# Kernel optimization log

Measured on AMD Instinct MI355X. Metric: run time of the kernel, lower is better.

Reference implementation:

```python
import jax, jax.numpy as jnp
import numpy as np

N_NODES = 500000
N_EDGES = 16000000
IN_DIM = 17


def setup_inputs() -> dict:
    key = jax.random.key(0)
    k1, k2, k3, k4, k5, k6, k7 = jax.random.split(key, 7)
    x = jax.random.normal(k1, (N_NODES, IN_DIM), dtype=jnp.float32)
    edge_index = jax.random.randint(k2, (2, N_EDGES), 0, N_NODES, dtype=jnp.int64)
    edge_weight = jax.random.uniform(k3, (N_EDGES,), dtype=jnp.float32)
    # SAGEConv(17, 1): lin_l applied to aggregated neighbors (with bias),
    # lin_r applied to root features (no bias, PyG convention).
    s = 1.0 / np.sqrt(IN_DIM)
    w_l = jax.random.uniform(k4, (1, IN_DIM), minval=-s, maxval=s, dtype=jnp.float32)
    b_l = jax.random.uniform(k5, (1,), minval=-s, maxval=s, dtype=jnp.float32)
    w_r = jax.random.uniform(k6, (1, IN_DIM), minval=-s, maxval=s, dtype=jnp.float32)
    # out: Linear(1, 1)
    k8, k9 = jax.random.split(k7)
    w_o = jax.random.uniform(k8, (1, 1), minval=-1.0, maxval=1.0, dtype=jnp.float32)
    b_o = jax.random.uniform(k9, (1,), minval=-1.0, maxval=1.0, dtype=jnp.float32)
    return {"x": x, "edge_index": edge_index, "edge_weight": edge_weight,
            "w_l": w_l, "b_l": b_l, "w_r": w_r, "w_o": w_o, "b_o": b_o}


def reference(x, edge_index, edge_weight, w_l, b_l, w_r, w_o, b_o):
    # SAGEConv (mean aggregation). edge_weight is unused (faithful to PyG SAGEConv).
    # Project to out_dim=1 BEFORE aggregation (linearity makes this exact and
    # avoids materializing a [E,17] gathered buffer):
    #   lin_l(mean_j x_j) + b_l == mean_j (x_j @ W_l^T) + b_l
    src, dst = edge_index[0], edge_index[1]
    x_proj_l = x @ w_l.T                      # [N, 1]
    msg = x_proj_l[src, 0]                    # [E]  gathered source projections
    agg = jax.ops.segment_sum(msg, dst, num_segments=x.shape[0])          # [N]
    cnt = jax.ops.segment_sum(jnp.ones_like(msg), dst, num_segments=x.shape[0])
    mean = agg / jnp.maximum(cnt, 1.0)        # zero for isolated nodes
    h = mean[:, None] + b_l + x @ w_r.T       # [N, 1]  lin_l(aggr) + lin_r(x)
    h = jax.nn.elu(h)
    return h @ w_o.T + b_o                    # [N, 1]
```

## Files before the change

### kernel.cpp

```cpp
#include <hip/hip_runtime.h>
#include <hip/hip_bf16.h>
#include <math.h>

#define IN_DIM 17
#define NB 128
#define LOG_BN 12
#define BN 4096
#define K_SPLIT 8
#define GRP 8
#define CHUNK 8192
#define EPT 32
#define VAL_SCALE 4096.0f
#define FP_SCALE 268435456.0f
#define FP_INV   (1.0 / 268435456.0)

__global__ void node_proj_kernel(const float* __restrict__ x,
                                 const float* __restrict__ w_l,
                                 const float* __restrict__ w_r,
                                 float* __restrict__ p_l,
                                 float* __restrict__ p_r,
                                 int n_nodes) {
    int i = blockIdx.x * blockDim.x + threadIdx.x;
    if (i >= n_nodes) return;
    const float* row = x + (size_t)i * IN_DIM;
    float sl = 0.0f, sr = 0.0f;
#pragma unroll
    for (int k = 0; k < IN_DIM; ++k) {
        float v = row[k];
        sl = fmaf(v, w_l[k], sl);
        sr = fmaf(v, w_r[k], sr);
    }
    p_l[i] = sl;
    p_r[i] = sr;
}

__global__ __launch_bounds__(256, 4)
void sort_scatter_kernel(const int* __restrict__ src,
                         const int* __restrict__ dst,
                         const float* __restrict__ p_l,
                         unsigned* __restrict__ staging,
                         unsigned short* __restrict__ segtab,
                         int n_edges) {
    __shared__ unsigned cnt[NB];
    __shared__ unsigned sstart[NB + 1];
    __shared__ unsigned lbuf[CHUNK];

    const int tid = threadIdx.x;
    const int blk = blockIdx.x;
    const int e0 = blk * CHUNK;
    const int chunk_n = min(CHUNK, n_edges - e0);
    const int nvec = chunk_n >> 2;

    for (int t = tid; t < NB; t += 256) cnt[t] = 0;
    __syncthreads();

    uint4 dreg[EPT / 4];
    uint4 sreg[EPT / 4];
    unsigned rpack[EPT / 2];
    const uint4* dv = (const uint4*)(dst + e0);
    const uint4* sv = (const uint4*)(src + e0);
#pragma unroll
    for (int k = 0; k < EPT / 4; ++k) {
        int q = tid + k * 256;
        if (q < nvec) {
            uint4 d = dv[q];
            dreg[k] = d;
            sreg[k] = sv[q];
            unsigned r0 = atomicAdd(&cnt[d.x >> LOG_BN], 1u);
            unsigned r1 = atomicAdd(&cnt[d.y >> LOG_BN], 1u);
            unsigned r2 = atomicAdd(&cnt[d.z >> LOG_BN], 1u);
            unsigned r3 = atomicAdd(&cnt[d.w >> LOG_BN], 1u);
            rpack[2 * k]     = r0 | (r1 << 16);
            rpack[2 * k + 1] = r2 | (r3 << 16);
        }
    }
    unsigned tail_rank = 0;
    {
        int i = (nvec << 2) + tid;
        if (i < chunk_n)
            tail_rank = atomicAdd(&cnt[(unsigned)dst[e0 + i] >> LOG_BN], 1u);
    }
    __syncthreads();

    if (tid < 64) {
        unsigned c0 = cnt[tid], c1 = cnt[tid + 64];
        unsigned s0 = c0;
#pragma unroll
        for (int off = 1; off < 64; off <<= 1) {
            unsigned v = __shfl_up(s0, off);
            if (tid >= off) s0 += v;
        }
        unsigned tot0 = __shfl(s0, 63);
        unsigned s1 = c1;
#pragma unroll
        for (int off = 1; off < 64; off <<= 1) {
            unsigned v = __shfl_up(s1, off);
            if (tid >= off) s1 += v;
        }
        s1 += tot0;
        sstart[tid + 1] = s0;
        sstart[tid + 65] = s1;
        if (tid == 0) sstart[0] = 0;
    }
    __syncthreads();

    for (int t = tid; t <= NB; t += 256)
        segtab[(size_t)blk * (NB + 2) + t] = (unsigned short)sstart[t];

#pragma unroll
    for (int k = 0; k < EPT / 4; ++k) {
        int q = tid + k * 256;
        if (q < nvec) {
            uint4 s = sreg[k];
            uint4 d = dreg[k];
            float pf[4] = {p_l[s.x], p_l[s.y], p_l[s.z], p_l[s.w]};
            unsigned dd[4] = {d.x, d.y, d.z, d.w};
            unsigned rk[4] = {rpack[2 * k] & 0xFFFFu, rpack[2 * k] >> 16,
                              rpack[2 * k + 1] & 0xFFFFu, rpack[2 * k + 1] >> 16};
#pragma unroll
            for (int u = 0; u < 4; ++u) {
                int fx = __float2int_rn(pf[u] * VAL_SCALE);
                fx = max(-32768, min(32767, fx));
                unsigned entry = ((unsigned)(fx & 0xFFFF) << 16) | (dd[u] & (BN - 1));
                unsigned b = dd[u] >> LOG_BN;
                lbuf[sstart[b] + rk[u]] = entry;
            }
        }
    }
    {
        int i = (nvec << 2) + tid;
        if (i < chunk_n) {
            unsigned s = (unsigned)src[e0 + i];
            unsigned d = (unsigned)dst[e0 + i];
            int fx = __float2int_rn(p_l[s] * VAL_SCALE);
            fx = max(-32768, min(32767, fx));
            unsigned entry = ((unsigned)(fx & 0xFFFF) << 16) | (d & (BN - 1));
            lbuf[sstart[d >> LOG_BN] + tail_rank] = entry;
        }
    }
    __syncthreads();

    uint4* outp = (uint4*)(staging + (size_t)blk * CHUNK);
    const uint4* lp = (const uint4*)lbuf;
    int nv4 = (chunk_n + 3) >> 2;
    for (int q = tid; q < nv4; q += 256)
        outp[q] = lp[q];
}

__global__ __launch_bounds__(256, 4)
void reduce_kernel(const unsigned* __restrict__ staging,
                   const unsigned short* __restrict__ segtab,
                   unsigned* __restrict__ bins,
                   int nblk) {
    __shared__ unsigned lds_p[BN];
    const int tid = threadIdx.x;
    const int b = blockIdx.x / K_SPLIT;
    const int j = blockIdx.x % K_SPLIT;
    const int grp = tid >> 3;
    const int sub = tid & (GRP - 1);

    for (int i = tid; i < BN; i += 256) lds_p[i] = 0u;
    __syncthreads();

    const int c0 = (int)((long long)nblk * j / K_SPLIT);
    const int c1 = (int)((long long)nblk * (j + 1) / K_SPLIT);

    int c = c0 + grp;
    unsigned s_nxt = 0, e_nxt = 0;
    if (c < c1) {
        const unsigned short* st = segtab + (size_t)c * (NB + 2) + b;
        s_nxt = st[0]; e_nxt = st[1];
    }
    while (c < c1) {
        unsigned s = s_nxt, e = e_nxt;
        const int cn = c + 32;
        if (cn < c1) {
            const unsigned short* st = segtab + (size_t)cn * (NB + 2) + b;
            s_nxt = st[0]; e_nxt = st[1];
        }
        const unsigned* sp = staging + (size_t)c * CHUNK;
        for (unsigned i = s + sub; i < e; i += GRP) {
            unsigned en = sp[i];
            int v = (int)(short)(en >> 16);
            atomicAdd(&lds_p[en & (BN - 1)], ((unsigned)v << 8) | 1u);
        }
        c = cn;
    }
    __syncthreads();
    unsigned* gb = bins + (size_t)b * BN;
    for (int i = tid; i < BN; i += 256) {
        unsigned v = lds_p[i];
        if (v) atomicAdd(&gb[i], v);
    }
}

__global__ void finalize_kernel(const float* __restrict__ p_r,
                                const unsigned* __restrict__ bins,
                                const float* __restrict__ b_l,
                                const float* __restrict__ w_o,
                                const float* __restrict__ b_o,
                                float* __restrict__ out,
                                int n_nodes) {
    int i = blockIdx.x * blockDim.x + threadIdx.x;
    if (i >= n_nodes) return;
    unsigned u = bins[i];
    int sum24 = ((int)u) >> 8;
    int cnt = (int)(u & 0xFFu);
    float sum = (float)sum24 * (1.0f / VAL_SCALE);
    float mean = sum / fmaxf((float)cnt, 1.0f);
    float h = mean + b_l[0] + p_r[i];
    h = (h > 0.0f) ? h : expm1f(h);
    out[i] = fmaf(h, w_o[0], b_o[0]);
}

__global__ void edge_scatter_fb(const int* __restrict__ edge_index,
                                const float* __restrict__ p_l,
                                unsigned long long* __restrict__ bins,
                                int n_edges) {
    int e = blockIdx.x * blockDim.x + threadIdx.x;
    if (e >= n_edges) return;
    int s = edge_index[e];
    int d = edge_index[n_edges + e];
    float p = p_l[s];
    long long sfx = (long long)llrintf(p * FP_SCALE);
    unsigned long long delta = ((unsigned long long)sfx << 20) | 1ULL;
    atomicAdd(&bins[d], delta);
}

__global__ void finalize_fb(const float* __restrict__ p_r,
                            const unsigned long long* __restrict__ bins,
                            const float* __restrict__ b_l,
                            const float* __restrict__ w_o,
                            const float* __restrict__ b_o,
                            float* __restrict__ out,
                            int n_nodes) {
    int i = blockIdx.x * blockDim.x + threadIdx.x;
    if (i >= n_nodes) return;
    long long packed = (long long)bins[i];
    int cntv = (int)(packed & 0xFFFFFLL);
    long long sfx = packed >> 20;
    float sum = (float)((double)sfx * FP_INV);
    float mean = sum / fmaxf((float)cntv, 1.0f);
    float h = mean + b_l[0] + p_r[i];
    h = (h > 0.0f) ? h : expm1f(h);
    out[i] = fmaf(h, w_o[0], b_o[0]);
}

static inline size_t align_up(size_t v, size_t a) { return (v + a - 1) & ~(a - 1); }

extern "C" void kernel_launch(void* const* d_in, const int* in_sizes, int n_in,
                              void* d_out, int out_size, void* d_ws, size_t ws_size,
                              hipStream_t stream) {
    const float* x   = (const float*)d_in[0];
    const int*   ei  = (const int*)d_in[1];
    const float* w_l = (const float*)d_in[3];
    const float* b_l = (const float*)d_in[4];
    const float* w_r = (const float*)d_in[5];
    const float* w_o = (const float*)d_in[6];
    const float* b_o = (const float*)d_in[7];
    float* out = (float*)d_out;

    const int n_nodes = in_sizes[0] / IN_DIM;
    const int n_edges = in_sizes[2];
    const int* src = ei;
    const int* dst = ei + n_edges;
    const int nblk = (n_edges + CHUNK - 1) / CHUNK;

    char* ws = (char*)d_ws;
    size_t off = 0;
    size_t o_pl = off;      off = align_up(off + (size_t)n_nodes * 4, 256);
    size_t o_pr = off;      off = align_up(off + (size_t)n_nodes * 4, 256);
    size_t o_stage = off;   off = align_up(off + (size_t)nblk * CHUNK * 4, 256);
    size_t o_seg = off;     off = align_up(off + (size_t)nblk * (NB + 2) * 2, 256);
    size_t o_bins = off;    off = align_up(off + (size_t)NB * BN * 4, 256);
    size_t need = off;

    float* p_l = (float*)(ws + o_pl);
    float* p_r = (float*)(ws + o_pr);

    const int B = 256;
    node_proj_kernel<<<(n_nodes + B - 1) / B, B, 0, stream>>>(x, w_l, w_r, p_l, p_r, n_nodes);

    if (ws_size >= need) {
        unsigned* staging       = (unsigned*)(ws + o_stage);
        unsigned short* segtab  = (unsigned short*)(ws + o_seg);
        unsigned* bins          = (unsigned*)(ws + o_bins);

        hipMemsetAsync(bins, 0, (size_t)NB * BN * 4, stream);
        sort_scatter_kernel<<<nblk, B, 0, stream>>>(src, dst, p_l, staging, segtab, n_edges);
        reduce_kernel<<<NB * K_SPLIT, B, 0, stream>>>(staging, segtab, bins, nblk);
        finalize_kernel<<<(n_nodes + B - 1) / B, B, 0, stream>>>(p_r, bins, b_l, w_o, b_o,
                                                                 out, n_nodes);
    } else {
        unsigned long long* bins_fb = (unsigned long long*)(ws + o_stage);
        hipMemsetAsync(bins_fb, 0, (size_t)n_nodes * 8, stream);
        edge_scatter_fb<<<(n_edges + B - 1) / B, B, 0, stream>>>(ei, p_l, bins_fb, n_edges);
        finalize_fb<<<(n_nodes + B - 1) / B, B, 0, stream>>>(p_r, bins_fb, b_l, w_o, b_o,
                                                             out, n_nodes);
    }
}
```

Measured before the change: 343.2 us.

## Split sort-scatter into separate histogram and scatter kernels

Splits the fused counting-sort kernel in two. A lightweight histogram kernel writes per-block bucket offsets to segtab, and a scatter kernel then reads them and claims slots with LDS atomics. This drops the per-edge rank registers and the in-kernel prefix scan from the scatter pass, which should lower register pressure. In exchange, dst is read twice from global memory and an extra launch is added.

```diff
diff --git a/kernel.cpp b/kernel.cpp
--- a/kernel.cpp
+++ b/kernel.cpp
@@ -34,16 +34,12 @@
     p_r[i] = sr;
 }
 
-__global__ __launch_bounds__(256, 4)
-void sort_scatter_kernel(const int* __restrict__ src,
-                         const int* __restrict__ dst,
-                         const float* __restrict__ p_l,
-                         unsigned* __restrict__ staging,
-                         unsigned short* __restrict__ segtab,
-                         int n_edges) {
-    __shared__ unsigned cnt[NB];
+__global__ __launch_bounds__(256, 8)
+void hist_kernel(const int* __restrict__ dst,
+                 unsigned short* __restrict__ segtab,
+                 int n_edges) {
+    __shared__ unsigned hist[NB];
     __shared__ unsigned sstart[NB + 1];
-    __shared__ unsigned lbuf[CHUNK];
 
     const int tid = threadIdx.x;
     const int blk = blockIdx.x;
@@ -51,39 +47,27 @@
     const int chunk_n = min(CHUNK, n_edges - e0);
     const int nvec = chunk_n >> 2;
 
-    for (int t = tid; t < NB; t += 256) cnt[t] = 0;
-    __syncthreads();
-
-    uint4 dreg[EPT / 4];
-    uint4 sreg[EPT / 4];
-    unsigned rpack[EPT / 2];
+    for (int t = tid; t < NB; t += 256) hist[t] = 0;
+    __syncthreads();
+
     const uint4* dv = (const uint4*)(dst + e0);
-    const uint4* sv = (const uint4*)(src + e0);
 #pragma unroll
     for (int k = 0; k < EPT / 4; ++k) {
         int q = tid + k * 256;
         if (q < nvec) {
             uint4 d = dv[q];
-            dreg[k] = d;
-            sreg[k] = sv[q];
-            unsigned r0 = atomicAdd(&cnt[d.x >> LOG_BN], 1u);
-            unsigned r1 = atomicAdd(&cnt[d.y >> LOG_BN], 1u);
-            unsigned r2 = atomicAdd(&cnt[d.z >> LOG_BN], 1u);
-            unsigned r3 = atomicAdd(&cnt[d.w >> LOG_BN], 1u);
-            rpack[2 * k]     = r0 | (r1 << 16);
-            rpack[2 * k + 1] = r2 | (r3 << 16);
-        }
-    }
-    unsigned tail_rank = 0;
-    {
-        int i = (nvec << 2) + tid;
-        if (i < chunk_n)
-            tail_rank = atomicAdd(&cnt[(unsigned)dst[e0 + i] >> LOG_BN], 1u);
-    }
+            atomicAdd(&hist[d.x >> LOG_BN], 1u);
+            atomicAdd(&hist[d.y >> LOG_BN], 1u);
+            atomicAdd(&hist[d.z >> LOG_BN], 1u);
+            atomicAdd(&hist[d.w >> LOG_BN], 1u);
+        }
+    }
+    for (int i = (nvec << 2) + tid; i < chunk_n; i += 256)
+        atomicAdd(&hist[(unsigned)dst[e0 + i] >> LOG_BN], 1u);
     __syncthreads();
 
     if (tid < 64) {
-        unsigned c0 = cnt[tid], c1 = cnt[tid + 64];
+        unsigned c0 = hist[tid], c1 = hist[tid + 64];
         unsigned s0 = c0;
 #pragma unroll
         for (int off = 1; off < 64; off <<= 1) {
@@ -106,7 +90,40 @@
 
     for (int t = tid; t <= NB; t += 256)
         segtab[(size_t)blk * (NB + 2) + t] = (unsigned short)sstart[t];
-
+}
+
+__global__ __launch_bounds__(256, 4)
+void scatter_kernel(const int* __restrict__ src,
+                    const int* __restrict__ dst,
+                    const float* __restrict__ p_l,
+                    const unsigned short* __restrict__ segtab,
+                    unsigned* __restrict__ staging,
+                    int n_edges) {
+    __shared__ unsigned pos[NB];
+    __shared__ unsigned lbuf[CHUNK];
+
+    const int tid = threadIdx.x;
+    const int blk = blockIdx.x;
+    const int e0 = blk * CHUNK;
+    const int chunk_n = min(CHUNK, n_edges - e0);
+    const int nvec = chunk_n >> 2;
+
+    for (int t = tid; t < NB; t += 256)
+        pos[t] = segtab[(size_t)blk * (NB + 2) + t];
+    __syncthreads();
+
+    uint4 dreg[EPT / 4];
+    uint4 sreg[EPT / 4];
+    const uint4* dv = (const uint4*)(dst + e0);
+    const uint4* sv = (const uint4*)(src + e0);
+#pragma unroll
+    for (int k = 0; k < EPT / 4; ++k) {
+        int q = tid + k * 256;
+        if (q < nvec) {
+            dreg[k] = dv[q];
+            sreg[k] = sv[q];
+        }
+    }
 #pragma unroll
     for (int k = 0; k < EPT / 4; ++k) {
         int q = tid + k * 256;
@@ -115,15 +132,14 @@
             uint4 d = dreg[k];
             float pf[4] = {p_l[s.x], p_l[s.y], p_l[s.z], p_l[s.w]};
             unsigned dd[4] = {d.x, d.y, d.z, d.w};
-            unsigned rk[4] = {rpack[2 * k] & 0xFFFFu, rpack[2 * k] >> 16,
-                              rpack[2 * k + 1] & 0xFFFFu, rpack[2 * k + 1] >> 16};
 #pragma unroll
             for (int u = 0; u < 4; ++u) {
                 int fx = __float2int_rn(pf[u] * VAL_SCALE);
                 fx = max(-32768, min(32767, fx));
                 unsigned entry = ((unsigned)(fx & 0xFFFF) << 16) | (dd[u] & (BN - 1));
                 unsigned b = dd[u] >> LOG_BN;
-                lbuf[sstart[b] + rk[u]] = entry;
+                unsigned p = atomicAdd(&pos[b], 1u);
+                lbuf[p] = entry;
             }
         }
     }
@@ -135,7 +151,8 @@
             int fx = __float2int_rn(p_l[s] * VAL_SCALE);
             fx = max(-32768, min(32767, fx));
             unsigned entry = ((unsigned)(fx & 0xFFFF) << 16) | (d & (BN - 1));
-            lbuf[sstart[d >> LOG_BN] + tail_rank] = entry;
+            unsigned p = atomicAdd(&pos[d >> LOG_BN], 1u);
+            lbuf[p] = entry;
         }
     }
     __syncthreads();
@@ -287,7 +304,8 @@
         unsigned* bins          = (unsigned*)(ws + o_bins);
 
         hipMemsetAsync(bins, 0, (size_t)NB * BN * 4, stream);
-        sort_scatter_kernel<<<nblk, B, 0, stream>>>(src, dst, p_l, staging, segtab, n_edges);
+        hist_kernel<<<nblk, B, 0, stream>>>(dst, segtab, n_edges);
+        scatter_kernel<<<nblk, B, 0, stream>>>(src, dst, p_l, segtab, staging, n_edges);
         reduce_kernel<<<NB * K_SPLIT, B, 0, stream>>>(staging, segtab, bins, nblk);
         finalize_kernel<<<(n_nodes + B - 1) / B, B, 0, stream>>>(p_r, bins, b_l, w_o, b_o,
                                                                  out, n_nodes);
```

Measured after the change: 355.1 us. 1.03x slower.
